# Kernel tuning notes

Measured on AMD Instinct MI355X. Metric: run time of the kernel, lower is better.

The kernel has to match this reference:

```python
import jax, jax.numpy as jnp
import numpy as np

B, D, E, H, TOP_K = 8192, 1024, 16, 1024, 8
LOSS_COEF = 0.01
NOISE_EPS = 0.01
INV_SQRT2 = 0.7071067811865476


def _normal_cdf(z):
    return 0.5 * (1.0 + jax.lax.erf(z * INV_SQRT2))


def _cv_squared(v):
    v = v.astype(jnp.float32)
    return jnp.var(v, ddof=1) / (jnp.mean(v) ** 2 + 1e-10)


def setup_inputs() -> dict:
    key = jax.random.key(0)
    k1, k2, k3, k4, k5, k6 = jax.random.split(key, 6)
    return {
        "x": jax.random.normal(k1, (B, D), dtype=jnp.float32),
        "w_gate": jax.random.normal(k2, (D, E), dtype=jnp.float32) * 0.02,
        "w_noise": jax.random.normal(k3, (D, E), dtype=jnp.float32) * 0.02,
        "expert_w": jax.random.normal(k4, (E, D, H), dtype=jnp.float32) * (1.0 / np.sqrt(D)),
        "expert_b": jax.random.normal(k5, (E, H), dtype=jnp.float32) * 0.01,
        "noise": jax.random.normal(k6, (B, E), dtype=jnp.float32),
    }


def reference(x, w_gate, w_noise, expert_w, expert_b, noise):
    # ---- noisy top-k gating (training=True) ----
    clean_logits = x @ w_gate                                   # [B, E]
    raw_noise_stddev = x @ w_noise                              # [B, E]
    noise_stddev = jax.nn.softplus(raw_noise_stddev) + NOISE_EPS
    noisy_logits = clean_logits + noise * noise_stddev          # [B, E]
    probs = jax.nn.softmax(noisy_logits, axis=1)                # [B, E]

    m = min(TOP_K + 1, E)
    top_logits, top_indices = jax.lax.top_k(probs, m)           # [B, m]
    top_k_logits = top_logits[:, :TOP_K]
    top_k_indices = top_indices[:, :TOP_K]
    top_k_gates = top_k_logits / (jnp.sum(top_k_logits, axis=1, keepdims=True) + 1e-6)

    rows = jnp.arange(B)[:, None]
    gates = jnp.zeros_like(probs).at[rows, top_k_indices].set(top_k_gates)  # [B, E]

    # ---- prob-in-top-k load (top_k < num_experts, training) ----
    # faithful to source: thresholds come from softmaxed top values,
    # compared against pre-softmax noisy/clean logits (as in original code)
    threshold_if_in = top_logits[:, TOP_K][:, None]             # [B, 1]
    threshold_if_out = top_logits[:, TOP_K - 1][:, None]        # [B, 1]
    is_in = noisy_logits > threshold_if_in
    prob_if_in = _normal_cdf((clean_logits - threshold_if_in) / noise_stddev)
    prob_if_out = _normal_cdf((clean_logits - threshold_if_out) / noise_stddev)
    load = jnp.where(is_in, prob_if_in, prob_if_out).sum(axis=0)  # [E]

    importance = gates.sum(axis=0)                              # [E]
    loss = LOSS_COEF * (_cv_squared(importance) + _cv_squared(load))

    # ---- experts: per-expert linear, gate-weighted sum over experts ----
    # y[b,h] = sum_e gates[b,e] * (x[b,:] @ W[e] + b[e])[h]
    y = jnp.einsum('bd,edh,be->bh', x, expert_w, gates) + gates @ expert_b
    return y, loss
```

## Files before the change

### kernel.cpp

```cpp
#include <hip/hip_runtime.h>
#include <cstdint>

#define B_SZ 8192
#define D_SZ 1024
#define E_SZ 16
#define H_SZ 1024
#define MAXTILES 544

using short8 = __attribute__((ext_vector_type(8))) short;
using f32x4  = __attribute__((ext_vector_type(4))) float;

__device__ __forceinline__ unsigned short f2bf(float f) {
  union { float f; unsigned int u; } v; v.f = f;
  unsigned int u = v.u;
  return (unsigned short)((u + 0x7fffu + ((u >> 16) & 1u)) >> 16);
}
__device__ __forceinline__ float bf2f(unsigned short h) {
  union { unsigned int u; float f; } v; v.u = ((unsigned int)h) << 16; return v.f;
}

__device__ __forceinline__ void async_ld16(void* lds, const void* g) {
  __builtin_amdgcn_global_load_lds(
      reinterpret_cast<const unsigned int __attribute__((address_space(1)))*>(
          reinterpret_cast<uintptr_t>(g)),
      reinterpret_cast<unsigned int __attribute__((address_space(3)))*>(
          reinterpret_cast<uintptr_t>(lds)),
      16, 0, 0);
}

__global__ __launch_bounds__(256) void prep(
    const float* __restrict__ x, const float* __restrict__ wg,
    const float* __restrict__ wn, const float* __restrict__ ew,
    unsigned short* __restrict__ xb, unsigned short* __restrict__ wtb,
    float* __restrict__ cl, float* __restrict__ rn, float* __restrict__ stats) {
  __shared__ __align__(16) char psm[16640];
  const int bx = blockIdx.x;
  const int tid = threadIdx.x;

  if (bx < 512) {
    float (*sx)[128] = (float(*)[128])psm;
    const int c  = tid & 31;
    const int rg = tid >> 5;
    const int rowbase = bx * 16;
    const float* wp = (c < 16) ? (wg + c) : (wn + (c - 16));
    float acc0 = 0.f, acc1 = 0.f;
    for (int ch = 0; ch < 8; ++ch) {
      __syncthreads();
      #pragma unroll
      for (int it = 0; it < 2; ++it) {
        const int idx = it * 256 + tid;
        const int r = idx >> 5, co = (idx & 31) * 4;
        *(float4*)&sx[r][co] =
            *(const float4*)(x + (size_t)(rowbase + r) * D_SZ + ch * 128 + co);
      }
      __syncthreads();
      #pragma unroll 4
      for (int d = 0; d < 128; ++d) {
        const float wv = wp[(size_t)(ch * 128 + d) * 16];
        acc0 = fmaf(sx[rg * 2][d],     wv, acc0);
        acc1 = fmaf(sx[rg * 2 + 1][d], wv, acc1);
      }
    }
    const int row0 = rowbase + rg * 2;
    if (c < 16) {
      cl[(size_t)row0 * 16 + c] = acc0;
      cl[(size_t)(row0 + 1) * 16 + c] = acc1;
    } else {
      rn[(size_t)row0 * 16 + (c - 16)] = acc0;
      rn[(size_t)(row0 + 1) * 16 + (c - 16)] = acc1;
    }
  } else if (bx < 4608) {
    const int b = bx - 512;
    const size_t i = (size_t)b * 256 + tid;
    const float4 v0 = ((const float4*)x)[2 * i];
    const float4 v1 = ((const float4*)x)[2 * i + 1];
    unsigned short r[8] = {f2bf(v0.x), f2bf(v0.y), f2bf(v0.z), f2bf(v0.w),
                           f2bf(v1.x), f2bf(v1.y), f2bf(v1.z), f2bf(v1.w)};
    ((short8*)xb)[i] = *(const short8*)r;
    if (b == 0 && tid < 48) stats[tid] = 0.0f;
  } else {
    float (*t)[65] = (float(*)[65])psm;
    const int b = bx - 4608;
    const int e  = b >> 8;
    const int d0 = ((b >> 4) & 15) * 64;
    const int h0 = (b & 15) * 64;
    const float* We = ew + (size_t)e * D_SZ * H_SZ;
    unsigned short* Wte = wtb + (size_t)e * D_SZ * H_SZ;
    #pragma unroll
    for (int i = 0; i < 4; ++i) {
      const int idx = i * 256 + tid;
      const int r = idx >> 4, co = (idx & 15) * 4;
      *(float4*)&t[r][co] =
          *(const float4*)(We + (size_t)(d0 + r) * H_SZ + h0 + co);
    }
    __syncthreads();
    #pragma unroll
    for (int i = 0; i < 2; ++i) {
      const int idx = i * 256 + tid;
      const int r = idx >> 3, c8 = (idx & 7) * 8;
      unsigned short v[8];
      #pragma unroll
      for (int j = 0; j < 8; ++j) v[j] = f2bf(t[c8 + j][r]);
      *(short8*)(Wte + (size_t)(h0 + r) * D_SZ + d0 + c8) = *(const short8*)v;
    }
  }
}

__global__ __launch_bounds__(64) void gating_post(
    const float* __restrict__ clg, const float* __restrict__ rng,
    const float* __restrict__ noise, float* __restrict__ gates,
    float* __restrict__ stats, int* __restrict__ rowidx, int* __restrict__ rowmap) {
  int* gcount = (int*)(stats + 32);
  __shared__ int lcnt[16];
  __shared__ int lbase[16];
  const int row = blockIdx.x * 64 + threadIdx.x;
  if (threadIdx.x < 16) lcnt[threadIdx.x] = 0;
  float cl[16], sd[16], nl[16], p[16];
  #pragma unroll
  for (int e = 0; e < 16; ++e) {
    cl[e] = clg[(size_t)row * 16 + e];
    const float r = rng[(size_t)row * 16 + e];
    sd[e] = fmaxf(r, 0.0f) + log1pf(expf(-fabsf(r))) + 0.01f;
    nl[e] = cl[e] + noise[(size_t)row * 16 + e] * sd[e];
  }
  float mx = nl[0];
  #pragma unroll
  for (int e = 1; e < 16; ++e) mx = fmaxf(mx, nl[e]);
  float sum = 0.0f;
  #pragma unroll
  for (int e = 0; e < 16; ++e) { p[e] = expf(nl[e] - mx); sum += p[e]; }
  const float inv = 1.0f / sum;
  #pragma unroll
  for (int e = 0; e < 16; ++e) p[e] *= inv;
  float tmp[16];
  #pragma unroll
  for (int e = 0; e < 16; ++e) tmp[e] = p[e];
  float tv[9]; int ti[9];
  for (int k = 0; k < 9; ++k) {
    float bv = tmp[0]; int bj = 0;
    #pragma unroll
    for (int j = 1; j < 16; ++j) if (tmp[j] > bv) { bv = tmp[j]; bj = j; }
    tv[k] = bv; ti[k] = bj; tmp[bj] = -1.0f;
  }
  float s8 = 0.0f;
  #pragma unroll
  for (int k = 0; k < 8; ++k) s8 += tv[k];
  const float denom = s8 + 1e-6f;
  float g[16];
  #pragma unroll
  for (int e = 0; e < 16; ++e) g[e] = 0.0f;
  for (int k = 0; k < 8; ++k) g[ti[k]] = tv[k] / denom;
  const float thr_in = tv[8], thr_out = tv[7];
  float lc[16];
  #pragma unroll
  for (int e = 0; e < 16; ++e) {
    const float t = (nl[e] > thr_in) ? thr_in : thr_out;
    lc[e] = 0.5f * (1.0f + erff(((cl[e] - t) / sd[e]) * 0.70710678118654752f));
  }
  #pragma unroll
  for (int e = 0; e < 16; ++e) gates[(size_t)row * 16 + e] = g[e];
  __syncthreads();
  int myslot[8];
  #pragma unroll
  for (int k = 0; k < 8; ++k) myslot[k] = atomicAdd(&lcnt[ti[k]], 1);
  __syncthreads();
  if (threadIdx.x < 16) lbase[threadIdx.x] = atomicAdd(&gcount[threadIdx.x], lcnt[threadIdx.x]);
  __syncthreads();
  #pragma unroll
  for (int k = 0; k < 8; ++k) {
    const int e = ti[k];
    const int slot = lbase[e] + myslot[k];
    rowidx[e * B_SZ + slot] = row;
    rowmap[row * 8 + k] = (e << 13) | slot;
  }
  #pragma unroll
  for (int e = 0; e < 16; ++e) {
    float vi = g[e], vl = lc[e];
    for (int o = 32; o > 0; o >>= 1) { vi += __shfl_down(vi, o); vl += __shfl_down(vl, o); }
    if (threadIdx.x == 0) {
      atomicAdd(&stats[e], vi);
      atomicAdd(&stats[16 + e], vl);
    }
  }
}

__global__ __launch_bounds__(256, 4) void moe_gemm(
    const unsigned short* __restrict__ Xb,
    const unsigned short* __restrict__ Wt,
    const float* __restrict__ gates,
    const float* __restrict__ ebias,
    const float* __restrict__ stats,
    const int* __restrict__ rowidx,
    unsigned short* __restrict__ partial) {
  __shared__ __align__(16) char smem[34816 + 512 + 512];
  unsigned short* sA = (unsigned short*)smem;
  unsigned short* sB = (unsigned short*)(smem + 16384);
  unsigned short* sOut = (unsigned short*)smem;
  float* sGG = (float*)(smem + 34816);
  int*   sRI = (int*)(smem + 34816 + 512);

  const int* gcount = (const int*)(stats + 32);
  int my_e = -1, tile = 0, tstart = 0, acc_t = 0;
  #pragma unroll
  for (int ee = 0; ee < 16; ++ee) {
    const int nt_e = (gcount[ee] + 127) >> 7;
    if (my_e < 0 && (int)blockIdx.y < acc_t + nt_e) {
      my_e = ee; tile = blockIdx.y - acc_t; tstart = acc_t;
    }
    acc_t += nt_e;
  }
  if (my_e < 0) return;
  const int e = my_e;
  const int slot0 = tile << 7;
  const int cnt = gcount[e];
  const int col0 = blockIdx.x << 7;
  const int pb = tstart << 7;

  const int tid  = threadIdx.x;
  const int lane = tid & 63;
  const int wave = tid >> 6;
  const int wm = wave >> 1, wn = wave & 1;
  const int ml = lane & 15;
  const int quad = lane >> 4;
  const int wbase = tid & ~63;

  if (tid < 128) {
    const int slot = slot0 + tid;
    const int ok = slot < cnt;
    const int row = ok ? rowidx[e * B_SZ + slot] : 0;
    sRI[tid] = row;
    sGG[tid] = ok ? gates[(size_t)row * 16 + e] : 0.0f;
  }
  float ebv[4];
  #pragma unroll
  for (int j = 0; j < 4; ++j)
    ebv[j] = ebias[(size_t)e * H_SZ + col0 + wn * 64 + j * 16 + ml];
  __syncthreads();

  const unsigned short* We = Wt + (size_t)e * D_SZ * H_SZ;
  const unsigned short* aptr[4];
  const unsigned short* bptr[4];
  #pragma unroll
  for (int i = 0; i < 4; ++i) {
    const int s = i * 256 + tid;
    const int m = s >> 3, pp = s & 7;
    const int gc = pp ^ (m & 7);
    aptr[i] = Xb + (size_t)sRI[m] * D_SZ + gc * 8;
    bptr[i] = We + (size_t)(col0 + m) * D_SZ + gc * 8;
  }

  f32x4 acc[4][4] = {};
  for (int kb = 0; kb < 16; ++kb) {
    const int k0 = kb * 64;
    __syncthreads();
    #pragma unroll
    for (int i = 0; i < 4; ++i)
      async_ld16(sA + (size_t)(i * 256 + wbase) * 8, aptr[i] + k0);
    #pragma unroll
    for (int i = 0; i < 4; ++i)
      async_ld16(sB + (size_t)(i * 256 + wbase) * 8, bptr[i] + k0);
    __syncthreads();
    #pragma unroll
    for (int kk = 0; kk < 2; ++kk) {
      short8 af[4], bfr[4];
      #pragma unroll
      for (int i = 0; i < 4; ++i) {
        const int m = wm * 64 + i * 16 + ml;
        const int cA = kk * 4 + quad;
        af[i]  = *(const short8*)(sA + ((size_t)m * 8 + (cA ^ (m & 7))) * 8);
        const int n = wn * 64 + i * 16 + ml;
        bfr[i] = *(const short8*)(sB + ((size_t)n * 8 + (cA ^ (n & 7))) * 8);
      }
      #pragma unroll
      for (int i = 0; i < 4; ++i)
        #pragma unroll
        for (int j = 0; j < 4; ++j)
          acc[i][j] = __builtin_amdgcn_mfma_f32_16x16x32_bf16(af[i], bfr[j], acc[i][j], 0, 0, 0);
    }
  }

  __syncthreads();
  #pragma unroll
  for (int i = 0; i < 4; ++i) {
    const int mbase = wm * 64 + i * 16 + quad * 4;
    #pragma unroll
    for (int r = 0; r < 4; ++r) {
      const int mrow = mbase + r;
      const float gv = sGG[mrow];
      #pragma unroll
      for (int j = 0; j < 4; ++j) {
        const int cc = wn * 64 + j * 16 + ml;
        sOut[mrow * 136 + cc] = f2bf(gv * (acc[i][j][r] + ebv[j]));
      }
    }
  }
  __syncthreads();
  const size_t prow0 = (size_t)(pb + slot0);
  #pragma unroll
  for (int it = 0; it < 8; ++it) {
    const int s = it * 256 + tid;
    const int rr = s >> 4;
    const int c8 = (s & 15) * 8;
    const short8 v = *(const short8*)(sOut + rr * 136 + c8);
    __builtin_nontemporal_store(
        v, (short8*)(partial + (prow0 + rr) * H_SZ + col0 + c8));
  }
}

__global__ __launch_bounds__(128) void reduce_k(
    const unsigned short* __restrict__ partial, const int* __restrict__ rowmap,
    const float* __restrict__ stats, float* __restrict__ y) {
  const int row = blockIdx.x;
  const int tid = threadIdx.x;
  const int* gcount = (const int*)(stats + 32);
  __shared__ int sp[8];
  if (tid < 8) {
    const int v = rowmap[row * 8 + tid];
    const int e = v >> 13, slot = v & 8191;
    int t = 0;
    #pragma unroll
    for (int ee = 0; ee < 16; ++ee) t += (ee < e) ? ((gcount[ee] + 127) >> 7) : 0;
    sp[tid] = (t << 7) + slot;
  }
  __syncthreads();
  const int c0 = tid * 8;
  float a[8] = {0.f, 0.f, 0.f, 0.f, 0.f, 0.f, 0.f, 0.f};
  #pragma unroll
  for (int k = 0; k < 8; ++k) {
    const short8 pv = *(const short8*)(partial + (size_t)sp[k] * H_SZ + c0);
    #pragma unroll
    for (int j = 0; j < 8; ++j) a[j] += bf2f((unsigned short)pv[j]);
  }
  float4 o0 = {a[0], a[1], a[2], a[3]};
  float4 o1 = {a[4], a[5], a[6], a[7]};
  *(float4*)(y + (size_t)row * H_SZ + c0)     = o0;
  *(float4*)(y + (size_t)row * H_SZ + c0 + 4) = o1;

  if (blockIdx.x == 0 && tid == 0) {
    double si = 0.0, sl = 0.0;
    for (int e = 0; e < 16; ++e) { si += stats[e]; sl += stats[16 + e]; }
    const double mi = si / 16.0, mld = sl / 16.0;
    double vi = 0.0, vl = 0.0;
    for (int e = 0; e < 16; ++e) {
      const double di = stats[e] - mi;       vi += di * di;
      const double dl = stats[16 + e] - mld; vl += dl * dl;
    }
    vi /= 15.0; vl /= 15.0;
    const double loss = 0.01 * (vi / (mi * mi + 1e-10) + vl / (mld * mld + 1e-10));
    y[(size_t)B_SZ * H_SZ] = (float)loss;
  }
}

extern "C" void kernel_launch(void* const* d_in, const int* in_sizes, int n_in,
                              void* d_out, int out_size, void* d_ws, size_t ws_size,
                              hipStream_t stream) {
  (void)in_sizes; (void)n_in; (void)out_size; (void)ws_size;
  const float* x    = (const float*)d_in[0];
  const float* wg   = (const float*)d_in[1];
  const float* wnoi = (const float*)d_in[2];
  const float* ew   = (const float*)d_in[3];
  const float* eb   = (const float*)d_in[4];
  const float* nz   = (const float*)d_in[5];
  float* y = (float*)d_out;

  char* ws = (char*)d_ws;
  const size_t MB = 1024 * 1024;
  unsigned short* xb     = (unsigned short*)(ws);
  unsigned short* wtb    = (unsigned short*)(ws + 16 * MB);
  float* cl              = (float*)(ws + 48 * MB);
  float* rn              = (float*)(ws + 48 * MB + 512 * 1024);
  float* gates           = (float*)(ws + 49 * MB);
  int*   rowidx          = (int*)  (ws + 49 * MB + 512 * 1024);
  int*   rowmap          = (int*)  (ws + 50 * MB);
  float* stats           = (float*)(ws + 50 * MB + 512 * 1024);
  unsigned short* partial= (unsigned short*)(ws + 52 * MB);

  hipLaunchKernelGGL(prep,        dim3(8704),        dim3(256), 0, stream,
                     x, wg, wnoi, ew, xb, wtb, cl, rn, stats);
  hipLaunchKernelGGL(gating_post, dim3(128),         dim3(64),  0, stream,
                     cl, rn, nz, gates, stats, rowidx, rowmap);
  hipLaunchKernelGGL(moe_gemm,    dim3(8, MAXTILES), dim3(256), 0, stream,
                     xb, wtb, gates, eb, stats, rowidx, partial);
  hipLaunchKernelGGL(reduce_k,    dim3(8192),        dim3(128), 0, stream,
                     partial, rowmap, stats, y);
}
```

Measured before the change: 476.9 us.

## Split expert GEMM and reduction into column slabs so partials stay in cache

The H dimension is split into four 256-column slabs. For each slab the expert GEMM writes a smaller partial buffer with ordinary (not nontemporal) stores, and a reduce kernel then combines it right away. The aim is to keep each slab's bf16 partial buffer (about 34 MB) resident in the large last-level cache instead of round-tripping the full buffer through HBM. The cost is eight launches instead of two, and the GEMM grid is smaller per launch, giving less parallelism and extra launch and tail overhead.

```diff
diff --git a/kernel.cpp b/kernel.cpp
--- a/kernel.cpp
+++ b/kernel.cpp
@@ -191,7 +191,8 @@
     const float* __restrict__ ebias,
     const float* __restrict__ stats,
     const int* __restrict__ rowidx,
-    unsigned short* __restrict__ partial) {
+    unsigned short* __restrict__ partial,
+    int col_slab) {
   __shared__ __align__(16) char smem[34816 + 512 + 512];
   unsigned short* sA = (unsigned short*)smem;
   unsigned short* sB = (unsigned short*)(smem + 16384);
@@ -213,7 +214,8 @@
   const int e = my_e;
   const int slot0 = tile << 7;
   const int cnt = gcount[e];
-  const int col0 = blockIdx.x << 7;
+  const int cs   = blockIdx.x << 7;
+  const int col0 = col_slab * 256 + cs;
   const int pb = tstart << 7;
 
   const int tid  = threadIdx.x;
@@ -302,41 +304,43 @@
     const int rr = s >> 4;
     const int c8 = (s & 15) * 8;
     const short8 v = *(const short8*)(sOut + rr * 136 + c8);
-    __builtin_nontemporal_store(
-        v, (short8*)(partial + (prow0 + rr) * H_SZ + col0 + c8));
-  }
-}
-
-__global__ __launch_bounds__(128) void reduce_k(
+    *(short8*)(partial + (prow0 + rr) * 256 + cs + c8) = v;
+  }
+}
+
+__global__ __launch_bounds__(256) void reduce_slab(
     const unsigned short* __restrict__ partial, const int* __restrict__ rowmap,
-    const float* __restrict__ stats, float* __restrict__ y) {
-  const int row = blockIdx.x;
+    const float* __restrict__ stats, float* __restrict__ y, int col_slab) {
+  const int row0 = blockIdx.x * 8;
   const int tid = threadIdx.x;
   const int* gcount = (const int*)(stats + 32);
-  __shared__ int sp[8];
-  if (tid < 8) {
-    const int v = rowmap[row * 8 + tid];
+  __shared__ int sp[8][8];
+  if (tid < 64) {
+    const int r = tid >> 3, k = tid & 7;
+    const int v = rowmap[(row0 + r) * 8 + k];
     const int e = v >> 13, slot = v & 8191;
     int t = 0;
     #pragma unroll
     for (int ee = 0; ee < 16; ++ee) t += (ee < e) ? ((gcount[ee] + 127) >> 7) : 0;
-    sp[tid] = (t << 7) + slot;
-  }
-  __syncthreads();
-  const int c0 = tid * 8;
+    sp[r][k] = (t << 7) + slot;
+  }
+  __syncthreads();
+  const int r = tid >> 5;
+  const int c = (tid & 31) * 8;
   float a[8] = {0.f, 0.f, 0.f, 0.f, 0.f, 0.f, 0.f, 0.f};
   #pragma unroll
   for (int k = 0; k < 8; ++k) {
-    const short8 pv = *(const short8*)(partial + (size_t)sp[k] * H_SZ + c0);
+    const short8 pv = *(const short8*)(partial + (size_t)sp[r][k] * 256 + c);
     #pragma unroll
     for (int j = 0; j < 8; ++j) a[j] += bf2f((unsigned short)pv[j]);
   }
   float4 o0 = {a[0], a[1], a[2], a[3]};
   float4 o1 = {a[4], a[5], a[6], a[7]};
-  *(float4*)(y + (size_t)row * H_SZ + c0)     = o0;
-  *(float4*)(y + (size_t)row * H_SZ + c0 + 4) = o1;
-
-  if (blockIdx.x == 0 && tid == 0) {
+  float* yp = y + (size_t)(row0 + r) * H_SZ + col_slab * 256 + c;
+  *(float4*)yp = o0;
+  *(float4*)(yp + 4) = o1;
+
+  if (col_slab == 0 && blockIdx.x == 0 && tid == 0) {
     double si = 0.0, sl = 0.0;
     for (int e = 0; e < 16; ++e) { si += stats[e]; sl += stats[16 + e]; }
     const double mi = si / 16.0, mld = sl / 16.0;
@@ -375,12 +379,14 @@
   float* stats           = (float*)(ws + 50 * MB + 512 * 1024);
   unsigned short* partial= (unsigned short*)(ws + 52 * MB);
 
-  hipLaunchKernelGGL(prep,        dim3(8704),        dim3(256), 0, stream,
+  hipLaunchKernelGGL(prep,        dim3(8704),      dim3(256), 0, stream,
                      x, wg, wnoi, ew, xb, wtb, cl, rn, stats);
-  hipLaunchKernelGGL(gating_post, dim3(128),         dim3(64),  0, stream,
+  hipLaunchKernelGGL(gating_post, dim3(128),       dim3(64),  0, stream,
                      cl, rn, nz, gates, stats, rowidx, rowmap);
-  hipLaunchKernelGGL(moe_gemm,    dim3(8, MAXTILES), dim3(256), 0, stream,
-                     xb, wtb, gates, eb, stats, rowidx, partial);
-  hipLaunchKernelGGL(reduce_k,    dim3(8192),        dim3(128), 0, stream,
-                     partial, rowmap, stats, y);
-}
+  for (int s = 0; s < 4; ++s) {
+    hipLaunchKernelGGL(moe_gemm,    dim3(2, MAXTILES), dim3(256), 0, stream,
+                       xb, wtb, gates, eb, stats, rowidx, partial, s);
+    hipLaunchKernelGGL(reduce_slab, dim3(1024),        dim3(256), 0, stream,
+                       partial, rowmap, stats, y, s);
+  }
+}
```

Result: slower. 511.1 us (+7.2%).

## Restructure gating logits GEMV with LDS-staged weights and batch reduce rows

Applied to the files above, without the earlier changes.

The gating-logit part of prep now uses 32-row blocks. Both w_gate and w_noise are staged transposed in LDS, and each thread accumulates 8 expert columns with vectorised LDS reads and a cross-half shuffle reduction, replacing per-thread scalar global weight loads. The reduce kernel now handles 4 rows per 256-thread block with 16 columns per thread, cutting block count and launch overhead. The prep grid and block offsets are adjusted to match. This adds LDS transpose writes that may bank-conflict, and fewer, larger blocks in both kernels.

```diff
diff --git a/kernel.cpp b/kernel.cpp
--- a/kernel.cpp
+++ b/kernel.cpp
@@ -33,44 +33,69 @@
     const float* __restrict__ wn, const float* __restrict__ ew,
     unsigned short* __restrict__ xb, unsigned short* __restrict__ wtb,
     float* __restrict__ cl, float* __restrict__ rn, float* __restrict__ stats) {
-  __shared__ __align__(16) char psm[16640];
+  __shared__ __align__(16) float psm[2 * 32 * 132];
   const int bx = blockIdx.x;
   const int tid = threadIdx.x;
 
-  if (bx < 512) {
-    float (*sx)[128] = (float(*)[128])psm;
-    const int c  = tid & 31;
-    const int rg = tid >> 5;
-    const int rowbase = bx * 16;
-    const float* wp = (c < 16) ? (wg + c) : (wn + (c - 16));
-    float acc0 = 0.f, acc1 = 0.f;
+  if (bx < 256) {
+    float* sx  = psm;
+    float* swT = psm + 32 * 132;
+    const int lane = tid & 63;
+    const int wave = tid >> 6;
+    const int row  = lane & 31;
+    const int half = lane >> 5;
+    const int rowbase = bx * 32;
+    float acc[8] = {0.f, 0.f, 0.f, 0.f, 0.f, 0.f, 0.f, 0.f};
+
+    const int srow = tid >> 3;
+    const int sd   = (tid & 7) * 16;
+    const int wd   = tid >> 1;
+    const int wc   = (tid & 1) * 16;
+    const float* wsrc = (wc == 0) ? wg : wn;
+
     for (int ch = 0; ch < 8; ++ch) {
       __syncthreads();
       #pragma unroll
-      for (int it = 0; it < 2; ++it) {
-        const int idx = it * 256 + tid;
-        const int r = idx >> 5, co = (idx & 31) * 4;
-        *(float4*)&sx[r][co] =
-            *(const float4*)(x + (size_t)(rowbase + r) * D_SZ + ch * 128 + co);
+      for (int k = 0; k < 4; ++k) {
+        const float4 v = *(const float4*)(
+            x + (size_t)(rowbase + srow) * D_SZ + ch * 128 + sd + k * 4);
+        *(float4*)&sx[srow * 132 + sd + k * 4] = v;
+      }
+      {
+        const float* wp = wsrc + (size_t)(ch * 128 + wd) * 16;
+        float wv[16];
+        #pragma unroll
+        for (int k = 0; k < 4; ++k)
+          *(float4*)&wv[k * 4] = *(const float4*)(wp + k * 4);
+        #pragma unroll
+        for (int j = 0; j < 16; ++j) swT[(wc + j) * 132 + wd] = wv[j];
       }
       __syncthreads();
       #pragma unroll 4
-      for (int d = 0; d < 128; ++d) {
-        const float wv = wp[(size_t)(ch * 128 + d) * 16];
-        acc0 = fmaf(sx[rg * 2][d],     wv, acc0);
-        acc1 = fmaf(sx[rg * 2 + 1][d], wv, acc1);
+      for (int dg = 0; dg < 16; ++dg) {
+        const int d = half * 64 + dg * 4;
+        const f32x4 xv = *(const f32x4*)&sx[row * 132 + d];
+        #pragma unroll
+        for (int c = 0; c < 8; ++c) {
+          const f32x4 wv = *(const f32x4*)&swT[(wave * 8 + c) * 132 + d];
+          acc[c] = fmaf(xv[0], wv[0], acc[c]);
+          acc[c] = fmaf(xv[1], wv[1], acc[c]);
+          acc[c] = fmaf(xv[2], wv[2], acc[c]);
+          acc[c] = fmaf(xv[3], wv[3], acc[c]);
+        }
       }
     }
-    const int row0 = rowbase + rg * 2;
-    if (c < 16) {
-      cl[(size_t)row0 * 16 + c] = acc0;
-      cl[(size_t)(row0 + 1) * 16 + c] = acc1;
-    } else {
-      rn[(size_t)row0 * 16 + (c - 16)] = acc0;
-      rn[(size_t)(row0 + 1) * 16 + (c - 16)] = acc1;
-    }
-  } else if (bx < 4608) {
-    const int b = bx - 512;
+    #pragma unroll
+    for (int c = 0; c < 8; ++c) acc[c] += __shfl_down(acc[c], 32);
+    if (lane < 32) {
+      const int cg = wave * 8;
+      float* dst = (cg < 16) ? (cl + (size_t)(rowbase + row) * 16 + cg)
+                             : (rn + (size_t)(rowbase + row) * 16 + (cg - 16));
+      *(float4*)dst = *(const float4*)&acc[0];
+      *(float4*)(dst + 4) = *(const float4*)&acc[4];
+    }
+  } else if (bx < 4352) {
+    const int b = bx - 256;
     const size_t i = (size_t)b * 256 + tid;
     const float4 v0 = ((const float4*)x)[2 * i];
     const float4 v1 = ((const float4*)x)[2 * i + 1];
@@ -80,7 +105,7 @@
     if (b == 0 && tid < 48) stats[tid] = 0.0f;
   } else {
     float (*t)[65] = (float(*)[65])psm;
-    const int b = bx - 4608;
+    const int b = bx - 4352;
     const int e  = b >> 8;
     const int d0 = ((b >> 4) & 15) * 64;
     const int h0 = (b & 15) * 64;
@@ -307,34 +332,45 @@
   }
 }
 
-__global__ __launch_bounds__(128) void reduce_k(
+__global__ __launch_bounds__(256) void reduce_k(
     const unsigned short* __restrict__ partial, const int* __restrict__ rowmap,
     const float* __restrict__ stats, float* __restrict__ y) {
-  const int row = blockIdx.x;
+  const int row0 = blockIdx.x * 4;
   const int tid = threadIdx.x;
   const int* gcount = (const int*)(stats + 32);
-  __shared__ int sp[8];
-  if (tid < 8) {
-    const int v = rowmap[row * 8 + tid];
+  __shared__ int sp[4][8];
+  if (tid < 32) {
+    const int r = tid >> 3, k = tid & 7;
+    const int v = rowmap[(row0 + r) * 8 + k];
     const int e = v >> 13, slot = v & 8191;
     int t = 0;
     #pragma unroll
     for (int ee = 0; ee < 16; ++ee) t += (ee < e) ? ((gcount[ee] + 127) >> 7) : 0;
-    sp[tid] = (t << 7) + slot;
-  }
-  __syncthreads();
-  const int c0 = tid * 8;
-  float a[8] = {0.f, 0.f, 0.f, 0.f, 0.f, 0.f, 0.f, 0.f};
+    sp[r][k] = (t << 7) + slot;
+  }
+  __syncthreads();
+  const int r = tid >> 6;
+  const int c0 = (tid & 63) * 16;
+  float a[16];
+  #pragma unroll
+  for (int j = 0; j < 16; ++j) a[j] = 0.f;
   #pragma unroll
   for (int k = 0; k < 8; ++k) {
-    const short8 pv = *(const short8*)(partial + (size_t)sp[k] * H_SZ + c0);
-    #pragma unroll
-    for (int j = 0; j < 8; ++j) a[j] += bf2f((unsigned short)pv[j]);
-  }
-  float4 o0 = {a[0], a[1], a[2], a[3]};
-  float4 o1 = {a[4], a[5], a[6], a[7]};
-  *(float4*)(y + (size_t)row * H_SZ + c0)     = o0;
-  *(float4*)(y + (size_t)row * H_SZ + c0 + 4) = o1;
+    const unsigned short* pp = partial + (size_t)sp[r][k] * H_SZ + c0;
+    const short8 p0 = *(const short8*)pp;
+    const short8 p1 = *(const short8*)(pp + 8);
+    #pragma unroll
+    for (int j = 0; j < 8; ++j) {
+      a[j]     += bf2f((unsigned short)p0[j]);
+      a[j + 8] += bf2f((unsigned short)p1[j]);
+    }
+  }
+  float* yp = y + (size_t)(row0 + r) * H_SZ + c0;
+  #pragma unroll
+  for (int q = 0; q < 4; ++q) {
+    float4 o = {a[q * 4], a[q * 4 + 1], a[q * 4 + 2], a[q * 4 + 3]};
+    *(float4*)(yp + q * 4) = o;
+  }
 
   if (blockIdx.x == 0 && tid == 0) {
     double si = 0.0, sl = 0.0;
@@ -375,12 +411,12 @@
   float* stats           = (float*)(ws + 50 * MB + 512 * 1024);
   unsigned short* partial= (unsigned short*)(ws + 52 * MB);
 
-  hipLaunchKernelGGL(prep,        dim3(8704),        dim3(256), 0, stream,
+  hipLaunchKernelGGL(prep,        dim3(8448),        dim3(256), 0, stream,
                      x, wg, wnoi, ew, xb, wtb, cl, rn, stats);
   hipLaunchKernelGGL(gating_post, dim3(128),         dim3(64),  0, stream,
                      cl, rn, nz, gates, stats, rowidx, rowmap);
   hipLaunchKernelGGL(moe_gemm,    dim3(8, MAXTILES), dim3(256), 0, stream,
                      xb, wtb, gates, eb, stats, rowidx, partial);
-  hipLaunchKernelGGL(reduce_k,    dim3(8192),        dim3(128), 0, stream,
+  hipLaunchKernelGGL(reduce_k,    dim3(2048),        dim3(256), 0, stream,
                      partial, rowmap, stats, y);
 }
```

Measured after the change: 407.0 us. 14.7% less time.
